# Kernel optimization log

Measured on AMD Instinct MI355X. Metric: run time of the kernel, lower is better.

The kernel has to match this reference:

```python
import jax, jax.numpy as jnp
import numpy as np
import math

D_MODEL = 512
H = 8
DK = D_MODEL // H  # 64
B, S = 2, 4096


def setup_inputs() -> dict:
    key = jax.random.key(0)
    ks = jax.random.split(key, 11)
    sc = 1.0 / math.sqrt(D_MODEL)
    return {
        "query": jax.random.normal(ks[0], (B, S, D_MODEL), jnp.float32),
        "key": jax.random.normal(ks[1], (B, S, D_MODEL), jnp.float32),
        "value": jax.random.normal(ks[2], (B, S, D_MODEL), jnp.float32),
        "Wq": jax.random.normal(ks[3], (D_MODEL, D_MODEL), jnp.float32) * sc,
        "bq": jnp.zeros((D_MODEL,), jnp.float32),
        "Wk": jax.random.normal(ks[4], (D_MODEL, D_MODEL), jnp.float32) * sc,
        "bk": jnp.zeros((D_MODEL,), jnp.float32),
        "Wv": jax.random.normal(ks[5], (D_MODEL, D_MODEL), jnp.float32) * sc,
        "bv": jnp.zeros((D_MODEL,), jnp.float32),
        "Wo": jax.random.normal(ks[6], (D_MODEL, D_MODEL), jnp.float32) * sc,
        "bo": jnp.zeros((D_MODEL,), jnp.float32),
    }


def reference(query, key, value, Wq, bq, Wk, bk, Wv, bv, Wo, bo):
    b = query.shape[0]
    # projections; W stored [in, out]
    def proj(x, W, bias):
        y = x @ W + bias                      # [B,S,h*dk]
        return y.reshape(b, -1, H, DK).transpose(0, 2, 1, 3)  # [B,h,S,dk]

    q = proj(query, Wq, bq)
    k = proj(key, Wk, bk)
    v = proj(value, Wv, bv)
    scores = jnp.einsum("bhqd,bhkd->bhqk", q, k) / math.sqrt(DK)
    attn = jax.nn.softmax(scores, axis=-1)    # [B,h,Sq,Sk]
    ctx = jnp.einsum("bhqk,bhkd->bhqd", attn, v)
    ctx = ctx.transpose(0, 2, 1, 3).reshape(b, -1, H * DK)  # [B,S,d_model]
    return ctx @ Wo + bo
```

## Files before the change

kernel.cpp:

```cpp
#include <hip/hip_runtime.h>
#include <hip/hip_bf16.h>

#define DM   512
#define HEADS 8
#define DKH  64
#define BATCH 2
#define SEQ  4096

typedef float  f32x4  __attribute__((ext_vector_type(4)));
typedef float  f32x16 __attribute__((ext_vector_type(16)));
typedef __bf16 bf16x8 __attribute__((ext_vector_type(8)));
typedef __bf16 bf16x4 __attribute__((ext_vector_type(4)));
typedef __bf16 bf16x2 __attribute__((ext_vector_type(2)));

static __device__ __forceinline__ f32x4 mfma16(bf16x8 a, bf16x8 b, f32x4 c) {
    return __builtin_amdgcn_mfma_f32_16x16x32_bf16(a, b, c, 0, 0, 0);
}
static __device__ __forceinline__ f32x16 mfma32(bf16x8 a, bf16x8 b, f32x16 c) {
    return __builtin_amdgcn_mfma_f32_32x32x16_bf16(a, b, c, 0, 0, 0);
}

#define GLD16(gp, lp) __builtin_amdgcn_global_load_lds( \
    (const __attribute__((address_space(1))) void*)(gp), \
    (__attribute__((address_space(3))) void*)(lp), 16, 0, 0)

struct WtAll { const float* W[4]; __bf16* Wt[4]; };

__global__ __launch_bounds__(256) void wt_convert_all(WtAll a) {
    const float* W = a.W[blockIdx.z];
    __bf16* Wt = a.Wt[blockIdx.z];
    __shared__ float tile[32][33];
    const int tx = threadIdx.x & 31, ty = threadIdx.x >> 5;
    const int nb = blockIdx.x * 32, kb = blockIdx.y * 32;
#pragma unroll
    for (int i = 0; i < 4; ++i)
        tile[ty + 8 * i][tx] = W[(size_t)(kb + ty + 8 * i) * DM + nb + tx];
    __syncthreads();
#pragma unroll
    for (int i = 0; i < 4; ++i)
        Wt[(size_t)(nb + ty + 8 * i) * DM + kb + tx] = (__bf16)tile[tx][ty + 8 * i];
}

struct Ptr3 { const void* A; const __bf16* Bt; const float* bias; void* Out; float ascale; };
struct GemmArgs { Ptr3 p[3]; };

template <bool A_FP32, bool OUT_BF16>
__global__ __launch_bounds__(256) void gemm_tile(GemmArgs args) {
    __shared__ __bf16 Al[128][72];
    __shared__ __bf16 Bl[128][72];
    const Ptr3 P = args.p[blockIdx.z];
    const int tid = threadIdx.x;
    const int lane = tid & 63, wid = tid >> 6;
    const int lq = lane & 15, hi = lane >> 4;
    const int m0 = blockIdx.x * 128, n0 = blockIdx.y * 128;
    const int wm = (wid >> 1) * 64, wn = (wid & 1) * 64;

    f32x4 acc[4][4] = {};

    for (int kt = 0; kt < DM / 64; ++kt) {
        const int k0 = kt * 64;
        bf16x8 abuf[4], bbuf[4];
        if (A_FP32) {
            const float* A = (const float*)P.A;
#pragma unroll
            for (int i = 0; i < 4; ++i) {
                int c = tid + 256 * i, row = c >> 3, cc = c & 7;
                const f32x4* src = (const f32x4*)&A[(size_t)(m0 + row) * DM + k0 + cc * 8];
                f32x4 f0 = src[0], f1 = src[1];
                bf16x8 v;
                v[0] = (__bf16)f0[0]; v[1] = (__bf16)f0[1]; v[2] = (__bf16)f0[2]; v[3] = (__bf16)f0[3];
                v[4] = (__bf16)f1[0]; v[5] = (__bf16)f1[1]; v[6] = (__bf16)f1[2]; v[7] = (__bf16)f1[3];
                abuf[i] = v;
            }
        } else {
            const __bf16* A = (const __bf16*)P.A;
#pragma unroll
            for (int i = 0; i < 4; ++i) {
                int c = tid + 256 * i, row = c >> 3, cc = c & 7;
                abuf[i] = *(const bf16x8*)&A[(size_t)(m0 + row) * DM + k0 + cc * 8];
            }
        }
        {
            const __bf16* Bt = P.Bt;
#pragma unroll
            for (int i = 0; i < 4; ++i) {
                int c = tid + 256 * i, row = c >> 3, cc = c & 7;
                bbuf[i] = *(const bf16x8*)&Bt[(size_t)(n0 + row) * DM + k0 + cc * 8];
            }
        }
        if (kt) __syncthreads();
#pragma unroll
        for (int i = 0; i < 4; ++i) {
            int c = tid + 256 * i, row = c >> 3, cc = c & 7;
            *(bf16x8*)&Al[row][cc * 8] = abuf[i];
            *(bf16x8*)&Bl[row][cc * 8] = bbuf[i];
        }
        __syncthreads();
#pragma unroll
        for (int ks = 0; ks < 2; ++ks) {
            bf16x8 af[4], bfv[4];
#pragma unroll
            for (int i = 0; i < 4; ++i)
                af[i] = *(const bf16x8*)&Al[wm + i * 16 + lq][ks * 32 + hi * 8];
#pragma unroll
            for (int j = 0; j < 4; ++j)
                bfv[j] = *(const bf16x8*)&Bl[wn + j * 16 + lq][ks * 32 + hi * 8];
#pragma unroll
            for (int i = 0; i < 4; ++i)
#pragma unroll
                for (int j = 0; j < 4; ++j)
                    acc[i][j] = mfma16(af[i], bfv[j], acc[i][j]);
        }
    }
    const float* bias = P.bias;
    const float asc = P.ascale;
#pragma unroll
    for (int j = 0; j < 4; ++j) {
        const int n = n0 + wn + j * 16 + lq;
        const float bv = bias[n];
#pragma unroll
        for (int i = 0; i < 4; ++i) {
#pragma unroll
            for (int r = 0; r < 4; ++r) {
                const int m = m0 + wm + i * 16 + hi * 4 + r;
                const float v = (acc[i][j][r] + bv) * asc;
                if (OUT_BF16) ((__bf16*)P.Out)[(size_t)m * DM + n] = (__bf16)v;
                else          ((float*)P.Out)[(size_t)m * DM + n] = v;
            }
        }
    }
}

__global__ __launch_bounds__(256) void v_transpose(const __bf16* __restrict__ Vp,
                                                   __bf16* __restrict__ Vt) {
    __shared__ __bf16 tile[64][72];
    const int tid = threadIdx.x;
    const int tt = blockIdx.x * 64;
    const int bh = blockIdx.y, b = bh >> 3, h = bh & 7;
#pragma unroll
    for (int i = 0; i < 2; ++i) {
        int c = tid + 256 * i, row = c >> 3, cc = c & 7;
        *(bf16x8*)&tile[row][cc * 8] =
            *(const bf16x8*)&Vp[(size_t)(b * SEQ + tt + row) * DM + h * DKH + cc * 8];
    }
    __syncthreads();
#pragma unroll
    for (int i = 0; i < 2; ++i) {
        int c = tid + 256 * i, row = c >> 3, cc = c & 7;
        bf16x8 v;
#pragma unroll
        for (int j = 0; j < 8; ++j) v[j] = tile[cc * 8 + j][row];
        *(bf16x8*)&Vt[(size_t)(bh * DKH + row) * SEQ + tt + cc * 8] = v;
    }
}

__global__ __launch_bounds__(256) void flash_attn2(const __bf16* __restrict__ Qp,
                                                   const __bf16* __restrict__ Kp,
                                                   const __bf16* __restrict__ Vt,
                                                   __bf16* __restrict__ Ctx) {
    __shared__ __bf16 Kl[2][64][64];
    __shared__ __bf16 Vl[2][64][64];
    __shared__ float  Lbuf[4][32];

    const int tid = threadIdx.x, lane = tid & 63, w = tid >> 6;
    const int c = lane & 31, h = lane >> 5;
    const int bh = blockIdx.y, b = bh >> 3, hd = bh & 7;
    const int qbase = blockIdx.x * 128 + w * 32;

    bf16x8 qf[4];
#pragma unroll
    for (int t = 0; t < 4; ++t)
        qf[t] = *(const bf16x8*)&Qp[(size_t)(b * SEQ + qbase + c) * DM + hd * DKH + 16 * t + 8 * h];

    const int r0 = w * 16 + (lane >> 3);
    const int r1 = r0 + 8;
    const int s0 = (lane & 7) ^ ((r0 ^ (r0 >> 3)) & 7);
    const int s1 = (lane & 7) ^ ((r1 ^ (r1 >> 3)) & 7);
    const __bf16* kg0 = Kp + (size_t)(b * SEQ + r0) * DM + hd * DKH + s0 * 8;
    const __bf16* kg1 = Kp + (size_t)(b * SEQ + r1) * DM + hd * DKH + s1 * 8;
    const __bf16* vg0 = Vt + (size_t)(bh * DKH + r0) * SEQ + s0 * 8;
    const __bf16* vg1 = Vt + (size_t)(bh * DKH + r1) * SEQ + s1 * 8;

    const int swz0 = (c ^ (c >> 3)) & 7;
    const int swz1 = ((32 + c) ^ ((32 + c) >> 3)) & 7;
    const int rowb0 = c * 128, rowb1 = (32 + c) * 128;
    const char* kb = (const char*)&Kl[0][0][0];
    const char* vb = (const char*)&Vl[0][0][0];

    f32x16 acc0 = {}, acc1 = {};
    float m_run = -__builtin_inff(), l_run = 0.f;

    GLD16(kg0, &Kl[0][w * 16][0]);
    GLD16(kg1, &Kl[0][w * 16 + 8][0]);
    GLD16(vg0, &Vl[0][w * 16][0]);
    GLD16(vg1, &Vl[0][w * 16 + 8][0]);
    __syncthreads();

    const int NT = SEQ / 64;
    for (int kvt = 0; kvt < NT; ++kvt) {
        const int cur = kvt & 1;
        if (kvt + 1 < NT) {
            const size_t ko = (size_t)(kvt + 1) * 64 * DM;
            const size_t vo = (size_t)(kvt + 1) * 64;
            GLD16(kg0 + ko, &Kl[cur ^ 1][w * 16][0]);
            GLD16(kg1 + ko, &Kl[cur ^ 1][w * 16 + 8][0]);
            GLD16(vg0 + vo, &Vl[cur ^ 1][w * 16][0]);
            GLD16(vg1 + vo, &Vl[cur ^ 1][w * 16 + 8][0]);
        }
        const char* kc = kb + cur * (64 * 128);
        const char* vc = vb + cur * (64 * 128);

        f32x16 sa = {}, sb = {};
        __builtin_amdgcn_s_setprio(1);
#pragma unroll
        for (int t = 0; t < 4; ++t) {
            bf16x8 kf0 = *(const bf16x8*)(kc + rowb0 + (((2 * t + h) ^ swz0) << 4));
            sa = mfma32(kf0, qf[t], sa);
            bf16x8 kf1 = *(const bf16x8*)(kc + rowb1 + (((2 * t + h) ^ swz1) << 4));
            sb = mfma32(kf1, qf[t], sb);
        }
        __builtin_amdgcn_s_setprio(0);

        float mx = sa[0];
#pragma unroll
        for (int r = 1; r < 16; ++r) mx = fmaxf(mx, sa[r]);
#pragma unroll
        for (int r = 0; r < 16; ++r) mx = fmaxf(mx, sb[r]);
        mx = fmaxf(mx, __shfl_xor(mx, 32));
        if (!__all(mx <= m_run + 8.f)) {
            const float mnew = fmaxf(m_run, mx);
            const float al = __builtin_amdgcn_exp2f(m_run - mnew);
            m_run = mnew;
            l_run *= al;
            if (lane < 32) Lbuf[w][lane] = al;
#pragma unroll
            for (int r = 0; r < 16; ++r) {
                const float a2 = Lbuf[w][(r & 3) + 8 * (r >> 2) + 4 * h];
                acc0[r] *= a2; acc1[r] *= a2;
            }
        }
        float ls = 0.f;
        float pa[16], pb[16];
#pragma unroll
        for (int r = 0; r < 16; ++r) { pa[r] = __builtin_amdgcn_exp2f(sa[r] - m_run); ls += pa[r]; }
#pragma unroll
        for (int r = 0; r < 16; ++r) { pb[r] = __builtin_amdgcn_exp2f(sb[r] - m_run); ls += pb[r]; }
        ls += __shfl_xor(ls, 32);
        l_run += ls;

        int ua[4][2], ub[4][2];
#pragma unroll
        for (int q4 = 0; q4 < 4; ++q4)
#pragma unroll
            for (int i = 0; i < 2; ++i) {
                bf16x2 ta; ta[0] = (__bf16)pa[4 * q4 + 2 * i]; ta[1] = (__bf16)pa[4 * q4 + 2 * i + 1];
                ua[q4][i] = __builtin_bit_cast(int, ta);
                bf16x2 tb; tb[0] = (__bf16)pb[4 * q4 + 2 * i]; tb[1] = (__bf16)pb[4 * q4 + 2 * i + 1];
                ub[q4][i] = __builtin_bit_cast(int, tb);
            }

#define EXCH(U, tl, W0, W1, W2, W3) do {                         \
            int z0 = h ? (U)[2*(tl)][0] : (U)[2*(tl)+1][0];      \
            int y0 = __shfl_xor(z0, 32);                         \
            W0 = h ? y0 : (U)[2*(tl)][0];                        \
            W2 = h ? (U)[2*(tl)+1][0] : y0;                      \
            int z1 = h ? (U)[2*(tl)][1] : (U)[2*(tl)+1][1];      \
            int y1 = __shfl_xor(z1, 32);                         \
            W1 = h ? y1 : (U)[2*(tl)][1];                        \
            W3 = h ? (U)[2*(tl)+1][1] : y1; } while (0)

#pragma unroll
        for (int tg = 0; tg < 4; ++tg) {
            int w0, w1, w2, w3;
            if (tg < 2) { EXCH(ua, tg, w0, w1, w2, w3); }
            else        { EXCH(ub, (tg - 2), w0, w1, w2, w3); }
            union { int i4[4]; bf16x8 v; } pf;
            pf.i4[0] = w0; pf.i4[1] = w1; pf.i4[2] = w2; pf.i4[3] = w3;
            bf16x8 vf0 = *(const bf16x8*)(vc + rowb0 + (((2 * tg + h) ^ swz0) << 4));
            bf16x8 vf1 = *(const bf16x8*)(vc + rowb1 + (((2 * tg + h) ^ swz1) << 4));
            __builtin_amdgcn_s_setprio(1);
            acc0 = mfma32(pf.v, vf0, acc0);
            acc1 = mfma32(pf.v, vf1, acc1);
            __builtin_amdgcn_s_setprio(0);
        }
#undef EXCH
        __syncthreads();
    }

    if (lane < 32) Lbuf[w][lane] = l_run;
    __bf16* outp = Ctx + (size_t)(b * SEQ + qbase) * DM + hd * DKH;
#pragma unroll
    for (int r = 0; r < 16; ++r) {
        const int qr = (r & 3) + 8 * (r >> 2) + 4 * h;
        const float li = 1.f / Lbuf[w][qr];
        outp[(size_t)qr * DM + c]      = (__bf16)(acc0[r] * li);
        outp[(size_t)qr * DM + 32 + c] = (__bf16)(acc1[r] * li);
    }
}

extern "C" void kernel_launch(void* const* d_in, const int* in_sizes, int n_in,
                              void* d_out, int out_size, void* d_ws, size_t ws_size,
                              hipStream_t stream) {
    (void)in_sizes; (void)n_in; (void)out_size;
    const float* query = (const float*)d_in[0];
    const float* key_  = (const float*)d_in[1];
    const float* value = (const float*)d_in[2];
    const float* Wq = (const float*)d_in[3];
    const float* bq = (const float*)d_in[4];
    const float* Wk = (const float*)d_in[5];
    const float* bk = (const float*)d_in[6];
    const float* Wv = (const float*)d_in[7];
    const float* bv = (const float*)d_in[8];
    const float* Wo = (const float*)d_in[9];
    const float* bo = (const float*)d_in[10];

    char* ws = (char*)d_ws;
    const size_t WSZ = (size_t)512 * 1024;
    const size_t XSZ = (size_t)8 * 1024 * 1024;
    if (ws_size < 4 * WSZ + 5 * XSZ) return;
    __bf16* Wtq = (__bf16*)(ws);
    __bf16* Wtk = (__bf16*)(ws + WSZ);
    __bf16* Wtv = (__bf16*)(ws + 2 * WSZ);
    __bf16* Wto = (__bf16*)(ws + 3 * WSZ);
    char* xb = ws + 4 * WSZ;
    __bf16* Qp  = (__bf16*)(xb);
    __bf16* Kp  = (__bf16*)(xb + XSZ);
    __bf16* Vp  = (__bf16*)(xb + 2 * XSZ);
    __bf16* Vt  = (__bf16*)(xb + 3 * XSZ);
    __bf16* Ctx = (__bf16*)(xb + 4 * XSZ);

    WtAll wa;
    wa.W[0] = Wq; wa.W[1] = Wk; wa.W[2] = Wv; wa.W[3] = Wo;
    wa.Wt[0] = Wtq; wa.Wt[1] = Wtk; wa.Wt[2] = Wtv; wa.Wt[3] = Wto;
    wt_convert_all<<<dim3(16, 16, 4), 256, 0, stream>>>(wa);

    const float QSC = 0.125f * 1.4426950408889634f;
    GemmArgs qa;
    qa.p[0] = {query, Wtq, bq, Qp, QSC};
    qa.p[1] = {key_,  Wtk, bk, Kp, 1.0f};
    qa.p[2] = {value, Wtv, bv, Vp, 1.0f};
    gemm_tile<true, true><<<dim3(64, 4, 3), 256, 0, stream>>>(qa);

    v_transpose<<<dim3(SEQ / 64, BATCH * HEADS), 256, 0, stream>>>(Vp, Vt);

    flash_attn2<<<dim3(SEQ / 128, BATCH * HEADS), 256, 0, stream>>>(Qp, Kp, Vt, Ctx);

    GemmArgs oa;
    oa.p[0] = {Ctx, Wto, bo, d_out, 1.0f};
    oa.p[1] = oa.p[0]; oa.p[2] = oa.p[0];
    gemm_tile<false, false><<<dim3(64, 4, 1), 256, 0, stream>>>(oa);
}
```

Baseline: 255.5 us.

## Split KV across two attention passes, pre-convert inputs, async-load GEMM tiles

Attention now splits the KV sequence in two along a grid z dimension, writing unnormalized partial outputs plus per-row max and sum, which a new combine kernel merges. This doubles the attention grid from 512 blocks, which is meant to fill more CUs on the device. Inputs are converted to bf16 in a separate kernel so the projection GEMM can use direct global-to-LDS loads, with the LDS padding removed and MFMA priority raised. The shuffle-based register exchange in attention is replaced by v_permlane32_swap. The trade-off is extra launches, partial-output traffic, and possible LDS bank conflicts from the unpadded tiles.

```diff
diff --git a/kernel.cpp b/kernel.cpp
--- a/kernel.cpp
+++ b/kernel.cpp
@@ -23,6 +23,20 @@
 #define GLD16(gp, lp) __builtin_amdgcn_global_load_lds( \
     (const __attribute__((address_space(1))) void*)(gp), \
     (__attribute__((address_space(3))) void*)(lp), 16, 0, 0)
+
+struct Cvt3 { const float* s[3]; __bf16* d[3]; };
+
+__global__ __launch_bounds__(256) void convert_x3(Cvt3 a) {
+    const float* s = a.s[blockIdx.y];
+    __bf16* d = a.d[blockIdx.y];
+    const size_t i = ((size_t)blockIdx.x * 256 + threadIdx.x) * 8;
+    f32x4 f0 = *(const f32x4*)&s[i];
+    f32x4 f1 = *(const f32x4*)&s[i + 4];
+    bf16x8 v;
+    v[0] = (__bf16)f0[0]; v[1] = (__bf16)f0[1]; v[2] = (__bf16)f0[2]; v[3] = (__bf16)f0[3];
+    v[4] = (__bf16)f1[0]; v[5] = (__bf16)f1[1]; v[6] = (__bf16)f1[2]; v[7] = (__bf16)f1[3];
+    *(bf16x8*)&d[i] = v;
+}
 
 struct WtAll { const float* W[4]; __bf16* Wt[4]; };
 
@@ -46,8 +60,8 @@
 
 template <bool A_FP32, bool OUT_BF16>
 __global__ __launch_bounds__(256) void gemm_tile(GemmArgs args) {
-    __shared__ __bf16 Al[128][72];
-    __shared__ __bf16 Bl[128][72];
+    __shared__ __bf16 Al[128][64];
+    __shared__ __bf16 Bl[128][64];
     const Ptr3 P = args.p[blockIdx.z];
     const int tid = threadIdx.x;
     const int lane = tid & 63, wid = tid >> 6;
@@ -55,47 +69,45 @@
     const int m0 = blockIdx.x * 128, n0 = blockIdx.y * 128;
     const int wm = (wid >> 1) * 64, wn = (wid & 1) * 64;
 
+    const int srow = wid * 32 + (lane >> 3);
+    const int scol = (lane & 7) * 8;
+    const __bf16* gb = P.Bt + (size_t)(n0 + srow) * DM + scol;
+    const __bf16* ga = (const __bf16*)P.A + (size_t)(m0 + srow) * DM + scol;
+
     f32x4 acc[4][4] = {};
 
     for (int kt = 0; kt < DM / 64; ++kt) {
         const int k0 = kt * 64;
-        bf16x8 abuf[4], bbuf[4];
+        if (kt) __syncthreads();
         if (A_FP32) {
             const float* A = (const float*)P.A;
+            bf16x8 abuf[4];
 #pragma unroll
             for (int i = 0; i < 4; ++i) {
-                int c = tid + 256 * i, row = c >> 3, cc = c & 7;
-                const f32x4* src = (const f32x4*)&A[(size_t)(m0 + row) * DM + k0 + cc * 8];
+                int cc = tid + 256 * i, row = cc >> 3, col = cc & 7;
+                const f32x4* src = (const f32x4*)&A[(size_t)(m0 + row) * DM + k0 + col * 8];
                 f32x4 f0 = src[0], f1 = src[1];
                 bf16x8 v;
                 v[0] = (__bf16)f0[0]; v[1] = (__bf16)f0[1]; v[2] = (__bf16)f0[2]; v[3] = (__bf16)f0[3];
                 v[4] = (__bf16)f1[0]; v[5] = (__bf16)f1[1]; v[6] = (__bf16)f1[2]; v[7] = (__bf16)f1[3];
                 abuf[i] = v;
             }
+#pragma unroll
+            for (int i = 0; i < 4; ++i) {
+                int cc = tid + 256 * i, row = cc >> 3, col = cc & 7;
+                *(bf16x8*)&Al[row][col * 8] = abuf[i];
+            }
         } else {
-            const __bf16* A = (const __bf16*)P.A;
-#pragma unroll
-            for (int i = 0; i < 4; ++i) {
-                int c = tid + 256 * i, row = c >> 3, cc = c & 7;
-                abuf[i] = *(const bf16x8*)&A[(size_t)(m0 + row) * DM + k0 + cc * 8];
-            }
-        }
-        {
-            const __bf16* Bt = P.Bt;
-#pragma unroll
-            for (int i = 0; i < 4; ++i) {
-                int c = tid + 256 * i, row = c >> 3, cc = c & 7;
-                bbuf[i] = *(const bf16x8*)&Bt[(size_t)(n0 + row) * DM + k0 + cc * 8];
-            }
-        }
-        if (kt) __syncthreads();
-#pragma unroll
-        for (int i = 0; i < 4; ++i) {
-            int c = tid + 256 * i, row = c >> 3, cc = c & 7;
-            *(bf16x8*)&Al[row][cc * 8] = abuf[i];
-            *(bf16x8*)&Bl[row][cc * 8] = bbuf[i];
-        }
+#pragma unroll
+            for (int i = 0; i < 4; ++i)
+                GLD16(ga + k0 + (size_t)i * 8 * DM, &Al[wid * 32 + i * 8][0]);
+        }
+#pragma unroll
+        for (int i = 0; i < 4; ++i)
+            GLD16(gb + k0 + (size_t)i * 8 * DM, &Bl[wid * 32 + i * 8][0]);
         __syncthreads();
+
+        __builtin_amdgcn_s_setprio(1);
 #pragma unroll
         for (int ks = 0; ks < 2; ++ks) {
             bf16x8 af[4], bfv[4];
@@ -111,6 +123,7 @@
                 for (int j = 0; j < 4; ++j)
                     acc[i][j] = mfma16(af[i], bfv[j], acc[i][j]);
         }
+        __builtin_amdgcn_s_setprio(0);
     }
     const float* bias = P.bias;
     const float asc = P.ascale;
@@ -154,10 +167,13 @@
     }
 }
 
-__global__ __launch_bounds__(256) void flash_attn2(const __bf16* __restrict__ Qp,
-                                                   const __bf16* __restrict__ Kp,
-                                                   const __bf16* __restrict__ Vt,
-                                                   __bf16* __restrict__ Ctx) {
+template <bool SPLIT>
+__global__ __launch_bounds__(256, 4) void flash_attn3(const __bf16* __restrict__ Qp,
+                                                      const __bf16* __restrict__ Kp,
+                                                      const __bf16* __restrict__ Vt,
+                                                      __bf16* __restrict__ O0,
+                                                      __bf16* __restrict__ O1,
+                                                      float2* __restrict__ ml) {
     __shared__ __bf16 Kl[2][64][64];
     __shared__ __bf16 Vl[2][64][64];
     __shared__ float  Lbuf[4][32];
@@ -166,6 +182,8 @@
     const int c = lane & 31, h = lane >> 5;
     const int bh = blockIdx.y, b = bh >> 3, hd = bh & 7;
     const int qbase = blockIdx.x * 128 + w * 32;
+    const int kvoff = SPLIT ? blockIdx.z * (SEQ / 2) : 0;
+    const int NT = SPLIT ? (SEQ / 2) / 64 : SEQ / 64;
 
     bf16x8 qf[4];
 #pragma unroll
@@ -176,10 +194,10 @@
     const int r1 = r0 + 8;
     const int s0 = (lane & 7) ^ ((r0 ^ (r0 >> 3)) & 7);
     const int s1 = (lane & 7) ^ ((r1 ^ (r1 >> 3)) & 7);
-    const __bf16* kg0 = Kp + (size_t)(b * SEQ + r0) * DM + hd * DKH + s0 * 8;
-    const __bf16* kg1 = Kp + (size_t)(b * SEQ + r1) * DM + hd * DKH + s1 * 8;
-    const __bf16* vg0 = Vt + (size_t)(bh * DKH + r0) * SEQ + s0 * 8;
-    const __bf16* vg1 = Vt + (size_t)(bh * DKH + r1) * SEQ + s1 * 8;
+    const __bf16* kg0 = Kp + (size_t)(b * SEQ + kvoff + r0) * DM + hd * DKH + s0 * 8;
+    const __bf16* kg1 = Kp + (size_t)(b * SEQ + kvoff + r1) * DM + hd * DKH + s1 * 8;
+    const __bf16* vg0 = Vt + (size_t)(bh * DKH + r0) * SEQ + kvoff + s0 * 8;
+    const __bf16* vg1 = Vt + (size_t)(bh * DKH + r1) * SEQ + kvoff + s1 * 8;
 
     const int swz0 = (c ^ (c >> 3)) & 7;
     const int swz1 = ((32 + c) ^ ((32 + c) >> 3)) & 7;
@@ -196,7 +214,6 @@
     GLD16(vg1, &Vl[0][w * 16 + 8][0]);
     __syncthreads();
 
-    const int NT = SEQ / 64;
     for (int kvt = 0; kvt < NT; ++kvt) {
         const int cur = kvt & 1;
         if (kvt + 1 < NT) {
@@ -259,23 +276,20 @@
                 ub[q4][i] = __builtin_bit_cast(int, tb);
             }
 
-#define EXCH(U, tl, W0, W1, W2, W3) do {                         \
-            int z0 = h ? (U)[2*(tl)][0] : (U)[2*(tl)+1][0];      \
-            int y0 = __shfl_xor(z0, 32);                         \
-            W0 = h ? y0 : (U)[2*(tl)][0];                        \
-            W2 = h ? (U)[2*(tl)+1][0] : y0;                      \
-            int z1 = h ? (U)[2*(tl)][1] : (U)[2*(tl)+1][1];      \
-            int y1 = __shfl_xor(z1, 32);                         \
-            W1 = h ? y1 : (U)[2*(tl)][1];                        \
-            W3 = h ? (U)[2*(tl)+1][1] : y1; } while (0)
-
 #pragma unroll
         for (int tg = 0; tg < 4; ++tg) {
-            int w0, w1, w2, w3;
-            if (tg < 2) { EXCH(ua, tg, w0, w1, w2, w3); }
-            else        { EXCH(ub, (tg - 2), w0, w1, w2, w3); }
+            int x0, y0, x1, y1;
+            if (tg < 2) {
+                x0 = ua[2 * tg][0]; y0 = ua[2 * tg + 1][0];
+                x1 = ua[2 * tg][1]; y1 = ua[2 * tg + 1][1];
+            } else {
+                x0 = ub[2 * (tg - 2)][0]; y0 = ub[2 * (tg - 2) + 1][0];
+                x1 = ub[2 * (tg - 2)][1]; y1 = ub[2 * (tg - 2) + 1][1];
+            }
+            asm("v_permlane32_swap_b32 %0, %1" : "+v"(x0), "+v"(y0));
+            asm("v_permlane32_swap_b32 %0, %1" : "+v"(x1), "+v"(y1));
             union { int i4[4]; bf16x8 v; } pf;
-            pf.i4[0] = w0; pf.i4[1] = w1; pf.i4[2] = w2; pf.i4[3] = w3;
+            pf.i4[0] = x0; pf.i4[1] = x1; pf.i4[2] = y0; pf.i4[3] = y1;
             bf16x8 vf0 = *(const bf16x8*)(vc + rowb0 + (((2 * tg + h) ^ swz0) << 4));
             bf16x8 vf1 = *(const bf16x8*)(vc + rowb1 + (((2 * tg + h) ^ swz1) << 4));
             __builtin_amdgcn_s_setprio(1);
@@ -283,19 +297,58 @@
             acc1 = mfma32(pf.v, vf1, acc1);
             __builtin_amdgcn_s_setprio(0);
         }
-#undef EXCH
         __syncthreads();
     }
 
-    if (lane < 32) Lbuf[w][lane] = l_run;
-    __bf16* outp = Ctx + (size_t)(b * SEQ + qbase) * DM + hd * DKH;
-#pragma unroll
-    for (int r = 0; r < 16; ++r) {
-        const int qr = (r & 3) + 8 * (r >> 2) + 4 * h;
-        const float li = 1.f / Lbuf[w][qr];
-        outp[(size_t)qr * DM + c]      = (__bf16)(acc0[r] * li);
-        outp[(size_t)qr * DM + 32 + c] = (__bf16)(acc1[r] * li);
-    }
+    if (SPLIT) {
+        __bf16* pp = blockIdx.z ? O1 : O0;
+#pragma unroll
+        for (int r = 0; r < 16; ++r) {
+            const int qr = (r & 3) + 8 * (r >> 2) + 4 * h;
+            const size_t off = (size_t)(b * SEQ + qbase + qr) * DM + hd * DKH;
+            pp[off + c]      = (__bf16)acc0[r];
+            pp[off + 32 + c] = (__bf16)acc1[r];
+        }
+        if (h == 0) {
+            float2 v; v.x = m_run; v.y = l_run;
+            ml[(size_t)(blockIdx.z * 16 + bh) * SEQ + qbase + c] = v;
+        }
+    } else {
+        if (lane < 32) Lbuf[w][lane] = l_run;
+        __bf16* outp = O0 + (size_t)(b * SEQ + qbase) * DM + hd * DKH;
+#pragma unroll
+        for (int r = 0; r < 16; ++r) {
+            const int qr = (r & 3) + 8 * (r >> 2) + 4 * h;
+            const float li = 1.f / Lbuf[w][qr];
+            outp[(size_t)qr * DM + c]      = (__bf16)(acc0[r] * li);
+            outp[(size_t)qr * DM + 32 + c] = (__bf16)(acc1[r] * li);
+        }
+    }
+}
+
+__global__ __launch_bounds__(256) void combine(const __bf16* __restrict__ P0,
+                                               const __bf16* __restrict__ P1,
+                                               const float2* __restrict__ ml,
+                                               __bf16* __restrict__ Ctx) {
+    const int row = blockIdx.x;
+    const int b = row >> 12, q = row & (SEQ - 1);
+    const int col = threadIdx.x * 2;
+    const int head = col >> 6;
+    const int bh = b * HEADS + head;
+    const float2 ml0 = ml[(size_t)bh * SEQ + q];
+    const float2 ml1 = ml[(size_t)(16 + bh) * SEQ + q];
+    const float m = fmaxf(ml0.x, ml1.x);
+    const float e0 = __builtin_amdgcn_exp2f(ml0.x - m);
+    const float e1 = __builtin_amdgcn_exp2f(ml1.x - m);
+    const float inv = 1.f / (ml0.y * e0 + ml1.y * e1);
+    const float f0 = e0 * inv, f1 = e1 * inv;
+    const size_t idx = (size_t)row * DM + col;
+    bf16x2 a = *(const bf16x2*)&P0[idx];
+    bf16x2 bb = *(const bf16x2*)&P1[idx];
+    bf16x2 o;
+    o[0] = (__bf16)((float)a[0] * f0 + (float)bb[0] * f1);
+    o[1] = (__bf16)((float)a[1] * f0 + (float)bb[1] * f1);
+    *(bf16x2*)&Ctx[idx] = o;
 }
 
 extern "C" void kernel_launch(void* const* d_in, const int* in_sizes, int n_in,
@@ -317,36 +370,78 @@
     char* ws = (char*)d_ws;
     const size_t WSZ = (size_t)512 * 1024;
     const size_t XSZ = (size_t)8 * 1024 * 1024;
-    if (ws_size < 4 * WSZ + 5 * XSZ) return;
+    const float QSC = 0.125f * 1.4426950408889634f;
+
     __bf16* Wtq = (__bf16*)(ws);
     __bf16* Wtk = (__bf16*)(ws + WSZ);
     __bf16* Wtv = (__bf16*)(ws + 2 * WSZ);
     __bf16* Wto = (__bf16*)(ws + 3 * WSZ);
     char* xb = ws + 4 * WSZ;
-    __bf16* Qp  = (__bf16*)(xb);
-    __bf16* Kp  = (__bf16*)(xb + XSZ);
-    __bf16* Vp  = (__bf16*)(xb + 2 * XSZ);
-    __bf16* Vt  = (__bf16*)(xb + 3 * XSZ);
-    __bf16* Ctx = (__bf16*)(xb + 4 * XSZ);
 
     WtAll wa;
     wa.W[0] = Wq; wa.W[1] = Wk; wa.W[2] = Wv; wa.W[3] = Wo;
     wa.Wt[0] = Wtq; wa.Wt[1] = Wtk; wa.Wt[2] = Wtv; wa.Wt[3] = Wto;
-    wt_convert_all<<<dim3(16, 16, 4), 256, 0, stream>>>(wa);
-
-    const float QSC = 0.125f * 1.4426950408889634f;
-    GemmArgs qa;
-    qa.p[0] = {query, Wtq, bq, Qp, QSC};
-    qa.p[1] = {key_,  Wtk, bk, Kp, 1.0f};
-    qa.p[2] = {value, Wtv, bv, Vp, 1.0f};
-    gemm_tile<true, true><<<dim3(64, 4, 3), 256, 0, stream>>>(qa);
-
-    v_transpose<<<dim3(SEQ / 64, BATCH * HEADS), 256, 0, stream>>>(Vp, Vt);
-
-    flash_attn2<<<dim3(SEQ / 128, BATCH * HEADS), 256, 0, stream>>>(Qp, Kp, Vt, Ctx);
-
-    GemmArgs oa;
-    oa.p[0] = {Ctx, Wto, bo, d_out, 1.0f};
-    oa.p[1] = oa.p[0]; oa.p[2] = oa.p[0];
-    gemm_tile<false, false><<<dim3(64, 4, 1), 256, 0, stream>>>(oa);
-}
+
+    if (ws_size >= 4 * WSZ + 7 * XSZ) {
+        __bf16* Qb = (__bf16*)(xb);
+        __bf16* Kb = (__bf16*)(xb + XSZ);
+        __bf16* Vb = (__bf16*)(xb + 2 * XSZ);
+        __bf16* Qp = (__bf16*)(xb + 3 * XSZ);
+        __bf16* Kp = (__bf16*)(xb + 4 * XSZ);
+        __bf16* Vp = (__bf16*)(xb + 5 * XSZ);
+        __bf16* Vt = (__bf16*)(xb + 6 * XSZ);
+        __bf16* Ctx = Vp;
+        __bf16* P0 = Qb;
+        __bf16* P1 = Kb;
+        float2* mlp = (float2*)Vb;
+
+        Cvt3 cv;
+        cv.s[0] = query; cv.s[1] = key_; cv.s[2] = value;
+        cv.d[0] = Qb; cv.d[1] = Kb; cv.d[2] = Vb;
+        convert_x3<<<dim3(2048, 3), 256, 0, stream>>>(cv);
+        wt_convert_all<<<dim3(16, 16, 4), 256, 0, stream>>>(wa);
+
+        GemmArgs qa;
+        qa.p[0] = {Qb, Wtq, bq, Qp, QSC};
+        qa.p[1] = {Kb, Wtk, bk, Kp, 1.0f};
+        qa.p[2] = {Vb, Wtv, bv, Vp, 1.0f};
+        gemm_tile<false, true><<<dim3(64, 4, 3), 256, 0, stream>>>(qa);
+
+        v_transpose<<<dim3(SEQ / 64, BATCH * HEADS), 256, 0, stream>>>(Vp, Vt);
+
+        flash_attn3<true><<<dim3(SEQ / 128, BATCH * HEADS, 2), 256, 0, stream>>>(
+            Qp, Kp, Vt, P0, P1, mlp);
+
+        combine<<<dim3(BATCH * SEQ), 256, 0, stream>>>(P0, P1, mlp, Ctx);
+
+        GemmArgs oa;
+        oa.p[0] = {Ctx, Wto, bo, d_out, 1.0f};
+        oa.p[1] = oa.p[0]; oa.p[2] = oa.p[0];
+        gemm_tile<false, false><<<dim3(64, 4, 1), 256, 0, stream>>>(oa);
+    } else {
+        if (ws_size < 4 * WSZ + 4 * XSZ) return;
+        __bf16* Qp = (__bf16*)(xb);
+        __bf16* Kp = (__bf16*)(xb + XSZ);
+        __bf16* Vp = (__bf16*)(xb + 2 * XSZ);
+        __bf16* Vt = (__bf16*)(xb + 3 * XSZ);
+        __bf16* Ctx = Vp;
+
+        wt_convert_all<<<dim3(16, 16, 4), 256, 0, stream>>>(wa);
+
+        GemmArgs qa;
+        qa.p[0] = {query, Wtq, bq, Qp, QSC};
+        qa.p[1] = {key_,  Wtk, bk, Kp, 1.0f};
+        qa.p[2] = {value, Wtv, bv, Vp, 1.0f};
+        gemm_tile<true, true><<<dim3(64, 4, 3), 256, 0, stream>>>(qa);
+
+        v_transpose<<<dim3(SEQ / 64, BATCH * HEADS), 256, 0, stream>>>(Vp, Vt);
+
+        flash_attn3<false><<<dim3(SEQ / 128, BATCH * HEADS, 1), 256, 0, stream>>>(
+            Qp, Kp, Vt, Ctx, nullptr, nullptr);
+
+        GemmArgs oa;
+        oa.p[0] = {Ctx, Wto, bo, d_out, 1.0f};
+        oa.p[1] = oa.p[0]; oa.p[2] = oa.p[0];
+        gemm_tile<false, false><<<dim3(64, 4, 1), 256, 0, stream>>>(oa);
+    }
+}
```

After: 251.4 us. No clear change (-1.6%).
